# Performance work log

Hardware: AMD Instinct MI355X
Metric: run time of the kernel (lower is better)

Reference implementation:

```python
import jax, jax.numpy as jnp
import numpy as np

TOP_K = 2
SCALE = 1.0  # score_scale_factor

def setup_inputs() -> dict:
    key = jax.random.key(0)
    ks = jax.random.split(key, 8)
    T, D, E, F = 4096, 1024, 8, 4096
    return {
        "hidden_states": jax.random.normal(ks[0], (T, D), jnp.float32),
        "gw1": jax.random.normal(ks[1], (D, D // 4), jnp.float32) * 0.02,
        "gb1": jnp.zeros((D // 4,), jnp.float32),
        "gw2": jax.random.normal(ks[2], (D // 4, D // 16), jnp.float32) * 0.02,
        "gb2": jnp.zeros((D // 16,), jnp.float32),
        "gw3": jax.random.normal(ks[3], (D // 16, E), jnp.float32) * 0.02,
        "w1": jax.random.normal(ks[4], (E, D, F), jnp.float32) * 0.02,
        "b1": jnp.zeros((E, F), jnp.float32),
        "w2": jax.random.normal(ks[5], (E, F, D), jnp.float32) * 0.02,
        "b2": jnp.zeros((E, D), jnp.float32),
    }

def reference(hidden_states, gw1, gb1, gw2, gb2, gw3, w1, b1, w2, b2):
    h = hidden_states                              # [T, D]
    g = jax.nn.relu(h @ gw1 + gb1)
    g = jax.nn.relu(g @ gw2 + gb2)
    router_logits = g @ gw3                        # [T, E]
    probs = jax.nn.softmax(router_logits.astype(jnp.float32), axis=-1)
    top_w, top_i = jax.lax.top_k(probs, TOP_K)     # [T, k]
    top_w = top_w / jnp.sum(top_w, axis=-1, keepdims=True)
    top_w = top_w.astype(h.dtype)
    T, E = router_logits.shape
    # combine weights: scatter normalized top-k weights into dense [T, E]
    cw = jnp.zeros((T, E), h.dtype).at[jnp.arange(T)[:, None], top_i].add(top_w)
    out = jnp.zeros_like(h)
    for e in range(E):  # small fixed expert count
        y = jax.nn.gelu(h @ w1[e] + b1[e]) @ w2[e] + b2[e]
        out = out + y * (cw[:, e:e + 1] * SCALE)
    return out, router_logits
```

## Files before the change

### kernel.cpp

```cpp
#include <hip/hip_runtime.h>
#include <stdint.h>

#define T_  4096
#define D_  1024
#define E_  8
#define F_  4096
#define H1_ 256
#define H2_ 64
#define SCALE_ 1.0f
#define NROW_ (2 * T_)
#define NTILES_ 72

typedef unsigned short ushort_t;
typedef unsigned int   uint32;
typedef __attribute__((ext_vector_type(8))) short  short8;
typedef __attribute__((ext_vector_type(4))) float  f32x4;
typedef __attribute__((ext_vector_type(8))) unsigned short us8;

__device__ __forceinline__ ushort_t f2bf(float f) {
  uint32 u = __float_as_uint(f);
  u += 0x7FFFu + ((u >> 16) & 1u);
  return (ushort_t)(u >> 16);
}
__device__ __forceinline__ float gelu_tanh(float x) {
  float u = 0.7978845608028654f * (x + 0.044715f * x * x * x);
  float e = __expf(2.0f * u);
  return 0.5f * x * (1.0f + (1.0f - 2.0f / (e + 1.0f)));
}
__device__ __forceinline__ void gll16(const void* gptr, void* lptr) {
  void* g = const_cast<void*>(gptr);
  __builtin_amdgcn_global_load_lds((__attribute__((address_space(1))) void*)g,
                                   (__attribute__((address_space(3))) void*)lptr,
                                   16, 0, 0);
}

__global__ void k_cvt_h(const float* __restrict__ h, ushort_t* __restrict__ hb) {
  int i = (blockIdx.x * 256 + threadIdx.x) * 8;
  float4 a = *(const float4*)(h + i);
  float4 b = *(const float4*)(h + i + 4);
  short8 v;
  v[0] = (short)f2bf(a.x); v[1] = (short)f2bf(a.y);
  v[2] = (short)f2bf(a.z); v[3] = (short)f2bf(a.w);
  v[4] = (short)f2bf(b.x); v[5] = (short)f2bf(b.y);
  v[6] = (short)f2bf(b.z); v[7] = (short)f2bf(b.w);
  *(short8*)(hb + i) = v;
}

__global__ void k_transpose_bf16(const float* __restrict__ in, ushort_t* __restrict__ out,
                                 int R, int C) {
  __shared__ float ltf[64][65];
  const size_t per = (size_t)R * C;
  const float* src = in + per * blockIdx.z;
  ushort_t* dst = out + per * blockIdx.z;
  int r0 = blockIdx.x * 64, c0 = blockIdx.y * 64;
  int tid = threadIdx.x;
  int cg = (tid & 15) * 4;
  int rr = tid >> 4;
#pragma unroll
  for (int rb = 0; rb < 64; rb += 16) {
    int r = rb + rr;
    float4 v = *(const float4*)(src + (size_t)(r0 + r) * C + c0 + cg);
    ltf[r][cg + 0] = v.x; ltf[r][cg + 1] = v.y;
    ltf[r][cg + 2] = v.z; ltf[r][cg + 3] = v.w;
  }
  __syncthreads();
  int c = tid >> 2, rch = (tid & 3) * 16;
  ushort_t tmp[16];
#pragma unroll
  for (int i = 0; i < 16; ++i) tmp[i] = f2bf(ltf[rch + i][c]);
  ushort_t* dp = dst + (size_t)(c0 + c) * R + r0 + rch;
  *(us8*)dp = *(const us8*)&tmp[0];
  *(us8*)(dp + 8) = *(const us8*)&tmp[8];
}

__global__ void k_router1(const float* __restrict__ h, const float* __restrict__ gw1,
                          double* __restrict__ p1) {
  __shared__ float sA[16][65];
  __shared__ float sB[16][65];
  int tx = threadIdx.x, ty = threadIdx.y;
  int tid = ty * 16 + tx;
  int m0 = blockIdx.y * 64, n0 = blockIdx.x * 64;
  int kc = blockIdx.z;
  double acc[4][4] = {};
  for (int k0 = kc * 256; k0 < kc * 256 + 256; k0 += 16) {
    {
      int m = tid & 63, kq = tid >> 6;
      float4 v = *(const float4*)(h + (size_t)(m0 + m) * D_ + k0 + kq * 4);
      sA[kq*4+0][m] = v.x; sA[kq*4+1][m] = v.y; sA[kq*4+2][m] = v.z; sA[kq*4+3][m] = v.w;
    }
    {
      int k = tid >> 4, nq = tid & 15;
      float4 v = *(const float4*)(gw1 + (size_t)(k0 + k) * H1_ + n0 + nq * 4);
      sB[k][nq*4+0] = v.x; sB[k][nq*4+1] = v.y; sB[k][nq*4+2] = v.z; sB[k][nq*4+3] = v.w;
    }
    __syncthreads();
#pragma unroll
    for (int k = 0; k < 16; ++k) {
      float a[4], b[4];
#pragma unroll
      for (int i = 0; i < 4; ++i) a[i] = sA[k][ty + i * 16];
#pragma unroll
      for (int j = 0; j < 4; ++j) b[j] = sB[k][tx * 4 + j];
#pragma unroll
      for (int i = 0; i < 4; ++i)
#pragma unroll
        for (int j = 0; j < 4; ++j)
          acc[i][j] += (double)a[i] * (double)b[j];
    }
    __syncthreads();
  }
  double* pd = p1 + (size_t)kc * T_ * H1_;
  for (int i = 0; i < 4; ++i)
    for (int j = 0; j < 4; ++j) {
      int m = m0 + ty + i * 16, n = n0 + tx * 4 + j;
      pd[(size_t)m * H1_ + n] = acc[i][j];
    }
}

__global__ void k_router23(const double* __restrict__ p1, const float* __restrict__ gb1,
                           const float* __restrict__ gw2, const float* __restrict__ gb2,
                           const float* __restrict__ gw3,
                           float* __restrict__ logits_out, int* __restrict__ tokExp,
                           float* __restrict__ tokW, int* __restrict__ counts) {
  __shared__ double sG1[4][256];
  __shared__ double sG2[4][64];
  __shared__ double sL[4][8];
  int lane = threadIdx.x & 63, wv = threadIdx.x >> 6;
  int t = blockIdx.x * 4 + wv;
  const size_t TH = (size_t)T_ * H1_;
  const double* gp = p1 + (size_t)t * H1_ + lane * 4;
  double s0 = 0, s1 = 0, s2 = 0, s3 = 0;
#pragma unroll
  for (int kc = 0; kc < 4; ++kc) {
    double2 va = *(const double2*)(gp + kc * TH);
    double2 vb = *(const double2*)(gp + kc * TH + 2);
    s0 += va.x; s1 += va.y; s2 += vb.x; s3 += vb.y;
  }
  int hbase = lane * 4;
  s0 += (double)gb1[hbase + 0]; s1 += (double)gb1[hbase + 1];
  s2 += (double)gb1[hbase + 2]; s3 += (double)gb1[hbase + 3];
  sG1[wv][hbase + 0] = s0 > 0.0 ? s0 : 0.0;
  sG1[wv][hbase + 1] = s1 > 0.0 ? s1 : 0.0;
  sG1[wv][hbase + 2] = s2 > 0.0 ? s2 : 0.0;
  sG1[wv][hbase + 3] = s3 > 0.0 ? s3 : 0.0;
  __syncthreads();
  double acc = (double)gb2[lane];
  for (int k = 0; k < H1_; ++k)
    acc += sG1[wv][k] * (double)gw2[k * H2_ + lane];
  sG2[wv][lane] = acc > 0.0 ? acc : 0.0;
  __syncthreads();
  if (lane < 8) {
    double l = 0.0;
    for (int j = 0; j < H2_; ++j) l += sG2[wv][j] * (double)gw3[j * E_ + lane];
    sL[wv][lane] = l;
    logits_out[(size_t)t * E_ + lane] = (float)l;
  }
  __syncthreads();
  if (lane == 0) {
    double best = -1e300, second = -1e300; int bi = 0, si = 0;
    for (int e = 0; e < E_; ++e) {
      double l = sL[wv][e];
      if (l > best)        { second = best; si = bi; best = l; bi = e; }
      else if (l > second) { second = l; si = e; }
    }
    double w0 = 1.0 / (1.0 + exp(second - best));
    tokExp[t*2]   = bi; tokExp[t*2+1] = si;
    tokW[t*2]     = (float)w0;
    tokW[t*2+1]   = (float)(1.0 - w0);
    atomicAdd(&counts[bi], 1);
    atomicAdd(&counts[si], 1);
  }
}

__global__ void k_assign(const int* __restrict__ tokExp, const int* __restrict__ counts,
                         int* cursor, int* __restrict__ list, int* __restrict__ rowOf,
                         int* __restrict__ tileTab) {
  int offs[E_];
  int s = 0;
#pragma unroll
  for (int e = 0; e < E_; ++e) { offs[e] = s; s += counts[e]; }
  if (blockIdx.x == 0 && threadIdx.x == 0) {
    int nt = 0;
    for (int e = 0; e < E_; ++e) {
      int cnt = counts[e];
      for (int m = 0; m * 128 < cnt; ++m) {
        tileTab[nt*3+0] = e;
        tileTab[nt*3+1] = offs[e] + m * 128;
        tileTab[nt*3+2] = (cnt - m * 128) < 128 ? (cnt - m * 128) : 128;
        ++nt;
      }
    }
    for (; nt < NTILES_; ++nt) tileTab[nt*3+0] = -1;
  }
  int t = blockIdx.x * 256 + threadIdx.x;
  for (int k = 0; k < 2; ++k) {
    int e = tokExp[t*2+k];
    int pos = atomicAdd(&cursor[e], 1);
    int row = offs[e] + pos;
    list[row] = t;
    rowOf[t*2+k] = row;
  }
}

__global__ __launch_bounds__(256) void k_moe_ffn1(
    const ushort_t* __restrict__ hb, const ushort_t* __restrict__ w1t,
    const float* __restrict__ b1, ushort_t* __restrict__ act,
    const int* __restrict__ list, const int* __restrict__ tileTab) {
  int ti = blockIdx.y;
  int e = tileTab[ti*3+0];
  if (e < 0) return;
  int rowStart = tileTab[ti*3+1];
  int cntTile  = tileTab[ti*3+2];
  int nBase = blockIdx.x * 128;
  const ushort_t* B = w1t + (size_t)e * F_ * D_;
  int tid = threadIdx.x, w = tid >> 6, lane = tid & 63;
  int m16 = lane & 15, kq = lane >> 4;
  __shared__ short8 lA[512];
  __shared__ short8 lB[512];
  int gr0 = rowStart + (w * 2) * 16 + m16;
  int gr1 = gr0 + 16;
  int t0 = list[min(gr0, NROW_ - 1)];
  int t1 = list[min(gr1, NROW_ - 1)];
  const ushort_t* aS0 = hb + (size_t)t0 * D_ + kq * 8;
  const ushort_t* aS1 = hb + (size_t)t1 * D_ + kq * 8;
  const ushort_t* bS0 = B + (size_t)(nBase + (w * 2) * 16 + m16) * D_ + kq * 8;
  const ushort_t* bS1 = bS0 + (size_t)16 * D_;
  short8* dA0 = &lA[(w * 2) * 64];
  short8* dA1 = &lA[(w * 2 + 1) * 64];
  short8* dB0 = &lB[(w * 2) * 64];
  short8* dB1 = &lB[(w * 2 + 1) * 64];
  int wr = w >> 1, wc = w & 1;
  f32x4 acc[4][4] = {};
  for (int k0 = 0; k0 < D_; k0 += 32) {
    gll16(aS0 + k0, dA0);
    gll16(aS1 + k0, dA1);
    gll16(bS0 + k0, dB0);
    gll16(bS1 + k0, dB1);
    __syncthreads();
    short8 af[4], bf4[4];
#pragma unroll
    for (int i = 0; i < 4; ++i) af[i] = lA[(wr * 4 + i) * 64 + lane];
#pragma unroll
    for (int j = 0; j < 4; ++j) bf4[j] = lB[(wc * 4 + j) * 64 + lane];
#pragma unroll
    for (int i = 0; i < 4; ++i)
#pragma unroll
      for (int j = 0; j < 4; ++j)
        acc[i][j] = __builtin_amdgcn_mfma_f32_16x16x32_bf16(af[i], bf4[j], acc[i][j], 0, 0, 0);
    __syncthreads();
  }
  const float* b1e = b1 + (size_t)e * F_;
  int quad = lane >> 4, cn = lane & 15;
#pragma unroll
  for (int i = 0; i < 4; ++i) {
    int lrow = (wr * 4 + i) * 16 + quad * 4;
#pragma unroll
    for (int r = 0; r < 4; ++r) {
      if (lrow + r < cntTile) {
        size_t gr = (size_t)rowStart + lrow + r;
#pragma unroll
        for (int j = 0; j < 4; ++j) {
          int n = nBase + (wc * 4 + j) * 16 + cn;
          float x = acc[i][j][r] + b1e[n];
          act[gr * F_ + n] = f2bf(gelu_tanh(x));
        }
      }
    }
  }
}

__global__ __launch_bounds__(256) void k_moe_ffn2(
    const ushort_t* __restrict__ act, const ushort_t* __restrict__ w2t,
    float* __restrict__ part, const int* __restrict__ tileTab) {
  int ti = blockIdx.y;
  int e = tileTab[ti*3+0];
  if (e < 0) return;
  int rowStart = tileTab[ti*3+1];
  int cntTile  = tileTab[ti*3+2];
  int kc = blockIdx.z;
  int nBase = blockIdx.x * 128;
  const ushort_t* B = w2t + (size_t)e * D_ * F_;
  int tid = threadIdx.x, w = tid >> 6, lane = tid & 63;
  int m16 = lane & 15, kq = lane >> 4;
  __shared__ short8 lA[512];
  __shared__ short8 lB[512];
  int gr0 = rowStart + (w * 2) * 16 + m16;
  int gr1 = gr0 + 16;
  const ushort_t* aS0 = act + (size_t)min(gr0, NROW_ - 1) * F_ + kq * 8;
  const ushort_t* aS1 = act + (size_t)min(gr1, NROW_ - 1) * F_ + kq * 8;
  const ushort_t* bS0 = B + (size_t)(nBase + (w * 2) * 16 + m16) * F_ + kq * 8;
  const ushort_t* bS1 = bS0 + (size_t)16 * F_;
  short8* dA0 = &lA[(w * 2) * 64];
  short8* dA1 = &lA[(w * 2 + 1) * 64];
  short8* dB0 = &lB[(w * 2) * 64];
  short8* dB1 = &lB[(w * 2 + 1) * 64];
  int wr = w >> 1, wc = w & 1;
  f32x4 acc[4][4] = {};
  int kBase = kc * (F_ / 2);
  for (int k0 = kBase; k0 < kBase + F_ / 2; k0 += 32) {
    gll16(aS0 + k0, dA0);
    gll16(aS1 + k0, dA1);
    gll16(bS0 + k0, dB0);
    gll16(bS1 + k0, dB1);
    __syncthreads();
    short8 af[4], bf4[4];
#pragma unroll
    for (int i = 0; i < 4; ++i) af[i] = lA[(wr * 4 + i) * 64 + lane];
#pragma unroll
    for (int j = 0; j < 4; ++j) bf4[j] = lB[(wc * 4 + j) * 64 + lane];
#pragma unroll
    for (int i = 0; i < 4; ++i)
#pragma unroll
      for (int j = 0; j < 4; ++j)
        acc[i][j] = __builtin_amdgcn_mfma_f32_16x16x32_bf16(af[i], bf4[j], acc[i][j], 0, 0, 0);
    __syncthreads();
  }
  float* pd = part + (size_t)kc * NROW_ * D_;
  int quad = lane >> 4, cn = lane & 15;
#pragma unroll
  for (int i = 0; i < 4; ++i) {
    int lrow = (wr * 4 + i) * 16 + quad * 4;
#pragma unroll
    for (int r = 0; r < 4; ++r) {
      if (lrow + r < cntTile) {
        size_t gr = (size_t)rowStart + lrow + r;
#pragma unroll
        for (int j = 0; j < 4; ++j) {
          int n = nBase + (wc * 4 + j) * 16 + cn;
          pd[gr * D_ + n] = acc[i][j][r];
        }
      }
    }
  }
}

__global__ void k_combine(const float* __restrict__ part, const int* __restrict__ rowOf,
                          const int* __restrict__ tokExp, const float* __restrict__ tokW,
                          const float* __restrict__ b2, float* __restrict__ out) {
  int t = blockIdx.x;
  int rA = rowOf[t*2], rB = rowOf[t*2+1];
  int eA = tokExp[t*2], eB = tokExp[t*2+1];
  float wA = tokW[t*2] * SCALE_, wB = tokW[t*2+1] * SCALE_;
  int d = threadIdx.x * 4;
  const size_t P = (size_t)NROW_ * D_;
  float4 a0 = *(const float4*)(part + (size_t)rA * D_ + d);
  float4 a1 = *(const float4*)(part + P + (size_t)rA * D_ + d);
  float4 b0 = *(const float4*)(part + (size_t)rB * D_ + d);
  float4 b1 = *(const float4*)(part + P + (size_t)rB * D_ + d);
  float4 ba = *(const float4*)(b2 + (size_t)eA * D_ + d);
  float4 bb = *(const float4*)(b2 + (size_t)eB * D_ + d);
  float4 o;
  o.x = wA * (a0.x + a1.x + ba.x) + wB * (b0.x + b1.x + bb.x);
  o.y = wA * (a0.y + a1.y + ba.y) + wB * (b0.y + b1.y + bb.y);
  o.z = wA * (a0.z + a1.z + ba.z) + wB * (b0.z + b1.z + bb.z);
  o.w = wA * (a0.w + a1.w + ba.w) + wB * (b0.w + b1.w + bb.w);
  *(float4*)(out + (size_t)t * D_ + d) = o;
}

extern "C" void kernel_launch(void* const* d_in, const int* in_sizes, int n_in,
                              void* d_out, int out_size, void* d_ws, size_t ws_size,
                              hipStream_t stream) {
  const float* h   = (const float*)d_in[0];
  const float* gw1 = (const float*)d_in[1];
  const float* gb1 = (const float*)d_in[2];
  const float* gw2 = (const float*)d_in[3];
  const float* gb2 = (const float*)d_in[4];
  const float* gw3 = (const float*)d_in[5];
  const float* w1  = (const float*)d_in[6];
  const float* b1  = (const float*)d_in[7];
  const float* w2  = (const float*)d_in[8];
  const float* b2  = (const float*)d_in[9];
  float* out    = (float*)d_out;
  float* logits = out + (size_t)T_ * D_;

  char* ws = (char*)d_ws;
  size_t o = 0;
  auto alloc = [&](size_t bytes) -> void* {
    o = (o + 255) & ~(size_t)255;
    void* p = ws + o;
    o += bytes;
    return p;
  };
  int*      counts  = (int*)alloc(2 * E_ * 4);
  int*      cursor  = counts + E_;
  int*      tileTab = (int*)alloc((size_t)NTILES_ * 3 * 4);
  int*      tokExp  = (int*)alloc((size_t)T_ * 2 * 4);
  float*    tokW    = (float*)alloc((size_t)T_ * 2 * 4);
  int*      list    = (int*)alloc((size_t)NROW_ * 4);
  int*      rowOf   = (int*)alloc((size_t)NROW_ * 4);
  ushort_t* hb      = (ushort_t*)alloc((size_t)T_ * D_ * 2);
  ushort_t* w2t     = (ushort_t*)alloc((size_t)E_ * D_ * F_ * 2);
  char*     bigA    = (char*)alloc((size_t)NROW_ * F_ * 2);
  double*   p1      = (double*)bigA;
  ushort_t* act     = (ushort_t*)bigA;
  char*     bigB    = (char*)alloc((size_t)E_ * D_ * F_ * 2);
  ushort_t* w1t     = (ushort_t*)bigB;
  float*    part    = (float*)bigB;
  (void)ws_size; (void)in_sizes; (void)n_in; (void)out_size;

  hipMemsetAsync(counts, 0, 2 * E_ * 4, stream);
  k_cvt_h<<<T_ * D_ / 2048, 256, 0, stream>>>(h, hb);
  k_transpose_bf16<<<dim3(D_ / 64, F_ / 64, E_), 256, 0, stream>>>(w1, w1t, D_, F_);
  k_transpose_bf16<<<dim3(F_ / 64, D_ / 64, E_), 256, 0, stream>>>(w2, w2t, F_, D_);
  k_router1<<<dim3(H1_ / 64, T_ / 64, 4), dim3(16, 16), 0, stream>>>(h, gw1, p1);
  k_router23<<<T_ / 4, 256, 0, stream>>>(p1, gb1, gw2, gb2, gw3, logits, tokExp, tokW, counts);
  k_assign<<<T_ / 256, 256, 0, stream>>>(tokExp, counts, cursor, list, rowOf, tileTab);
  k_moe_ffn1<<<dim3(F_ / 128, NTILES_), 256, 0, stream>>>(hb, w1t, b1, act, list, tileTab);
  k_moe_ffn2<<<dim3(D_ / 128, NTILES_, 2), 256, 0, stream>>>(act, w2t, part, tileTab);
  k_combine<<<T_, 256, 0, stream>>>(part, rowOf, tokExp, tokW, b2, out);
}
```

Measured before the change: 932.3 us.

## Double-buffer LDS tiles in MoE FFN GEMMs to overlap loads with MFMA

Both expert FFN kernels now use two LDS buffers for the A and B tiles. The next K-slice is issued via global_load_lds before computing on the current one, and a partial vmcnt wait lets the previous stage's loads complete while newer ones stay in flight. This is meant to hide global-memory latency behind the MFMA work instead of stalling on every K step. It doubles LDS use per block, which may reduce occupancy, and it relies on hand-placed waitcnt and barriers being correct.

```diff
diff --git a/kernel.cpp b/kernel.cpp
--- a/kernel.cpp
+++ b/kernel.cpp
@@ -17,6 +17,9 @@
 typedef __attribute__((ext_vector_type(4))) float  f32x4;
 typedef __attribute__((ext_vector_type(8))) unsigned short us8;
 
+#define BARRIER() do { asm volatile("" ::: "memory"); __builtin_amdgcn_s_barrier(); asm volatile("" ::: "memory"); } while (0)
+#define WAITVM(N) asm volatile("s_waitcnt vmcnt(" #N ")" ::: "memory")
+
 __device__ __forceinline__ ushort_t f2bf(float f) {
   uint32 u = __float_as_uint(f);
   u += 0x7FFFu + ((u >> 16) & 1u);
@@ -32,6 +35,29 @@
   __builtin_amdgcn_global_load_lds((__attribute__((address_space(1))) void*)g,
                                    (__attribute__((address_space(3))) void*)lptr,
                                    16, 0, 0);
+}
+
+__device__ __forceinline__ void stage4(const ushort_t* a0, const ushort_t* a1,
+                                       const ushort_t* b0, const ushort_t* b1,
+                                       short8* An, short8* Bn, int w) {
+  gll16(a0, An + (w * 2 + 0) * 64);
+  gll16(a1, An + (w * 2 + 1) * 64);
+  gll16(b0, Bn + (w * 2 + 0) * 64);
+  gll16(b1, Bn + (w * 2 + 1) * 64);
+}
+
+__device__ __forceinline__ void mfma_step(const short8* Ac, const short8* Bc,
+                                          int wr, int wc, int lane, f32x4 acc[4][4]) {
+  short8 af[4], bf4[4];
+#pragma unroll
+  for (int i = 0; i < 4; ++i) af[i] = Ac[(wr * 4 + i) * 64 + lane];
+#pragma unroll
+  for (int j = 0; j < 4; ++j) bf4[j] = Bc[(wc * 4 + j) * 64 + lane];
+#pragma unroll
+  for (int i = 0; i < 4; ++i)
+#pragma unroll
+    for (int j = 0; j < 4; ++j)
+      acc[i][j] = __builtin_amdgcn_mfma_f32_16x16x32_bf16(af[i], bf4[j], acc[i][j], 0, 0, 0);
 }
 
 __global__ void k_cvt_h(const float* __restrict__ h, ushort_t* __restrict__ hb) {
@@ -215,8 +241,8 @@
   const ushort_t* B = w1t + (size_t)e * F_ * D_;
   int tid = threadIdx.x, w = tid >> 6, lane = tid & 63;
   int m16 = lane & 15, kq = lane >> 4;
-  __shared__ short8 lA[512];
-  __shared__ short8 lB[512];
+  __shared__ short8 lA[2][512];
+  __shared__ short8 lB[2][512];
   int gr0 = rowStart + (w * 2) * 16 + m16;
   int gr1 = gr0 + 16;
   int t0 = list[min(gr0, NROW_ - 1)];
@@ -225,30 +251,26 @@
   const ushort_t* aS1 = hb + (size_t)t1 * D_ + kq * 8;
   const ushort_t* bS0 = B + (size_t)(nBase + (w * 2) * 16 + m16) * D_ + kq * 8;
   const ushort_t* bS1 = bS0 + (size_t)16 * D_;
-  short8* dA0 = &lA[(w * 2) * 64];
-  short8* dA1 = &lA[(w * 2 + 1) * 64];
-  short8* dB0 = &lB[(w * 2) * 64];
-  short8* dB1 = &lB[(w * 2 + 1) * 64];
   int wr = w >> 1, wc = w & 1;
   f32x4 acc[4][4] = {};
-  for (int k0 = 0; k0 < D_; k0 += 32) {
-    gll16(aS0 + k0, dA0);
-    gll16(aS1 + k0, dA1);
-    gll16(bS0 + k0, dB0);
-    gll16(bS1 + k0, dB1);
-    __syncthreads();
-    short8 af[4], bf4[4];
-#pragma unroll
-    for (int i = 0; i < 4; ++i) af[i] = lA[(wr * 4 + i) * 64 + lane];
-#pragma unroll
-    for (int j = 0; j < 4; ++j) bf4[j] = lB[(wc * 4 + j) * 64 + lane];
-#pragma unroll
-    for (int i = 0; i < 4; ++i)
-#pragma unroll
-      for (int j = 0; j < 4; ++j)
-        acc[i][j] = __builtin_amdgcn_mfma_f32_16x16x32_bf16(af[i], bf4[j], acc[i][j], 0, 0, 0);
-    __syncthreads();
-  }
+  short8* Ac = lA[0]; short8* An = lA[1];
+  short8* Bc = lB[0]; short8* Bn = lB[1];
+  stage4(aS0, aS1, bS0, bS1, Ac, Bc, w);
+  const int NSTEP = D_ / 32;
+  for (int step = 0; step < NSTEP - 1; ++step) {
+    int k0 = (step + 1) * 32;
+    stage4(aS0 + k0, aS1 + k0, bS0 + k0, bS1 + k0, An, Bn, w);
+    WAITVM(4);
+    BARRIER();
+    mfma_step(Ac, Bc, wr, wc, lane, acc);
+    BARRIER();
+    short8* t;
+    t = Ac; Ac = An; An = t;
+    t = Bc; Bc = Bn; Bn = t;
+  }
+  WAITVM(0);
+  BARRIER();
+  mfma_step(Ac, Bc, wr, wc, lane, acc);
   const float* b1e = b1 + (size_t)e * F_;
   int quad = lane >> 4, cn = lane & 15;
 #pragma unroll
@@ -279,42 +301,38 @@
   int cntTile  = tileTab[ti*3+2];
   int kc = blockIdx.z;
   int nBase = blockIdx.x * 128;
-  const ushort_t* B = w2t + (size_t)e * D_ * F_;
+  const ushort_t* Bw = w2t + (size_t)e * D_ * F_;
   int tid = threadIdx.x, w = tid >> 6, lane = tid & 63;
   int m16 = lane & 15, kq = lane >> 4;
-  __shared__ short8 lA[512];
-  __shared__ short8 lB[512];
+  __shared__ short8 lA[2][512];
+  __shared__ short8 lB[2][512];
   int gr0 = rowStart + (w * 2) * 16 + m16;
   int gr1 = gr0 + 16;
-  const ushort_t* aS0 = act + (size_t)min(gr0, NROW_ - 1) * F_ + kq * 8;
-  const ushort_t* aS1 = act + (size_t)min(gr1, NROW_ - 1) * F_ + kq * 8;
-  const ushort_t* bS0 = B + (size_t)(nBase + (w * 2) * 16 + m16) * F_ + kq * 8;
+  int kBase = kc * (F_ / 2);
+  const ushort_t* aS0 = act + (size_t)min(gr0, NROW_ - 1) * F_ + kBase + kq * 8;
+  const ushort_t* aS1 = act + (size_t)min(gr1, NROW_ - 1) * F_ + kBase + kq * 8;
+  const ushort_t* bS0 = Bw + (size_t)(nBase + (w * 2) * 16 + m16) * F_ + kBase + kq * 8;
   const ushort_t* bS1 = bS0 + (size_t)16 * F_;
-  short8* dA0 = &lA[(w * 2) * 64];
-  short8* dA1 = &lA[(w * 2 + 1) * 64];
-  short8* dB0 = &lB[(w * 2) * 64];
-  short8* dB1 = &lB[(w * 2 + 1) * 64];
   int wr = w >> 1, wc = w & 1;
   f32x4 acc[4][4] = {};
-  int kBase = kc * (F_ / 2);
-  for (int k0 = kBase; k0 < kBase + F_ / 2; k0 += 32) {
-    gll16(aS0 + k0, dA0);
-    gll16(aS1 + k0, dA1);
-    gll16(bS0 + k0, dB0);
-    gll16(bS1 + k0, dB1);
-    __syncthreads();
-    short8 af[4], bf4[4];
-#pragma unroll
-    for (int i = 0; i < 4; ++i) af[i] = lA[(wr * 4 + i) * 64 + lane];
-#pragma unroll
-    for (int j = 0; j < 4; ++j) bf4[j] = lB[(wc * 4 + j) * 64 + lane];
-#pragma unroll
-    for (int i = 0; i < 4; ++i)
-#pragma unroll
-      for (int j = 0; j < 4; ++j)
-        acc[i][j] = __builtin_amdgcn_mfma_f32_16x16x32_bf16(af[i], bf4[j], acc[i][j], 0, 0, 0);
-    __syncthreads();
-  }
+  short8* Ac = lA[0]; short8* An = lA[1];
+  short8* Bc = lB[0]; short8* Bn = lB[1];
+  stage4(aS0, aS1, bS0, bS1, Ac, Bc, w);
+  const int NSTEP = (F_ / 2) / 32;
+  for (int step = 0; step < NSTEP - 1; ++step) {
+    int k0 = (step + 1) * 32;
+    stage4(aS0 + k0, aS1 + k0, bS0 + k0, bS1 + k0, An, Bn, w);
+    WAITVM(4);
+    BARRIER();
+    mfma_step(Ac, Bc, wr, wc, lane, acc);
+    BARRIER();
+    short8* t;
+    t = Ac; Ac = An; An = t;
+    t = Bc; Bc = Bn; Bn = t;
+  }
+  WAITVM(0);
+  BARRIER();
+  mfma_step(Ac, Bc, wr, wc, lane, acc);
   float* pd = part + (size_t)kc * NROW_ * D_;
   int quad = lane >> 4, cn = lane & 15;
 #pragma unroll
```

After: 890.2 us. -4.5%, faster.
